# Kernel optimization log

Hardware: AMD Instinct MI355X
Metric: run time of the kernel (lower is better)

The kernel has to match this reference:

```python
import jax, jax.numpy as jnp
import numpy as np

B, N, L = 1, 512, 384
D_IN, D_OUT, HEADS, D_FF = 128, 64, 4, 256
EPS = 1e-5


def layer_norm(x, g, b):
    m = jnp.mean(x, axis=-1, keepdims=True)
    v = jnp.mean((x - m) ** 2, axis=-1, keepdims=True)
    return g * (x - m) / jnp.sqrt(v + EPS) + b


def setup_inputs() -> dict:
    key = jax.random.key(0)
    ks = jax.random.split(key, 10)
    s = 0.05
    return {
        "src": jax.random.normal(ks[0], (B, L, L, D_IN), jnp.float32),
        "tgt": jax.random.normal(ks[1], (B, N, L, D_OUT), jnp.float32),
        "Wp": jax.random.normal(ks[2], (D_IN, HEADS), jnp.float32) * s,
        "bp": jnp.zeros((HEADS,), jnp.float32),
        "Wm": jax.random.normal(ks[3], (D_OUT, D_OUT), jnp.float32) * s,
        "bm": jnp.zeros((D_OUT,), jnp.float32),
        "Wo": jax.random.normal(ks[4], (D_OUT, D_OUT), jnp.float32) * s,
        "bo": jnp.zeros((D_OUT,), jnp.float32),
        "W1": jax.random.normal(ks[5], (D_OUT, D_FF), jnp.float32) * s,
        "b1": jnp.zeros((D_FF,), jnp.float32),
        "W2": jax.random.normal(ks[6], (D_FF, D_OUT), jnp.float32) * s,
        "b2": jnp.zeros((D_OUT,), jnp.float32),
        "g_norm": jnp.ones((D_IN,), jnp.float32),
        "bt_norm": jnp.zeros((D_IN,), jnp.float32),
        "g1": jnp.ones((D_OUT,), jnp.float32),
        "bt1": jnp.zeros((D_OUT,), jnp.float32),
        "g2": jnp.ones((D_OUT,), jnp.float32),
        "bt2": jnp.zeros((D_OUT,), jnp.float32),
    }


def reference(src, tgt, Wp, bp, Wm, bm, Wo, bo, W1, b1, W2, b2,
              g_norm, bt_norm, g1, bt1, g2, bt2):
    H = HEADS
    C = D_OUT // H  # channels per head group
    # symmetrize pair features over the two residue axes
    src = 0.5 * (src + jnp.swapaxes(src, 1, 2))
    src = layer_norm(src, g_norm, bt_norm)
    tgt2 = layer_norm(tgt, g1, bt1)
    # attention map from pair features; softmax over the FIRST residue axis (dim=1)
    attn = jax.nn.softmax(src @ Wp + bp, axis=1)          # [B, L(k), L(l), H]
    # value projection of MSA, split channels into (C, H) matching view(B,-1,H,N,L)
    v = (tgt2 @ Wm + bm).reshape(B, N, L, C, H)           # [B, N, L(k), C, H]
    # out[b,n,l,c,h] = sum_k v[b,n,k,c,h] * attn[b,k,l,h]
    o = jnp.einsum('bnkch,bklh->bnlch', v, attn).reshape(B, N, L, D_OUT)
    tgt2 = o @ Wo + bo
    tgt = tgt + tgt2
    # norm2 (view to (B*N,L,-1) is irrelevant: LN acts on last dim) + FFN
    tgt2 = layer_norm(tgt, g2, bt2)
    tgt2 = jax.nn.relu(tgt2 @ W1 + b1) @ W2 + b2
    return tgt + tgt2
```

## Files before the change

### kernel.cpp

```cpp
#include <hip/hip_runtime.h>
#include <math.h>

#define LL 384
#define NN 512
#define DIN 128
#define DOUT 64
#define HH 4
#define CC 16
#define DFF 256
#define EPS 1e-5f

typedef __attribute__((ext_vector_type(4))) float f32x4;
typedef __attribute__((ext_vector_type(8))) short bf16x8;

__device__ __forceinline__ short f2bf(float f) {
    union { float f; unsigned u; } v; v.f = f;
    unsigned r = v.u + 0x7fff + ((v.u >> 16) & 1);
    return (short)(r >> 16);
}
#define MFMA16(a, b, c) __builtin_amdgcn_mfma_f32_16x16x32_bf16(a, b, c, 0, 0, 0)

__global__ __launch_bounds__(256) void k1_logits(
    const float* __restrict__ src, const float* __restrict__ Wp,
    const float* __restrict__ bp, const float* __restrict__ g_norm,
    const float* __restrict__ bt_norm, float* __restrict__ logits)
{
    int k = blockIdx.x;
    int wave = threadIdx.x >> 6;
    int lane = threadIdx.x & 63;
    int l = blockIdx.y * 4 + wave;
    if (k > l) return;
    const float* r1 = src + ((size_t)k * LL + l) * DIN;
    const float* r2 = src + ((size_t)l * LL + k) * DIN;
    float2 a = *(const float2*)(r1 + lane * 2);
    float2 b = *(const float2*)(r2 + lane * 2);
    float x0 = 0.5f * (a.x + b.x);
    float x1 = 0.5f * (a.y + b.y);
    float s = x0 + x1, ss = x0 * x0 + x1 * x1;
    #pragma unroll
    for (int m = 1; m < 64; m <<= 1) { s += __shfl_xor(s, m); ss += __shfl_xor(ss, m); }
    float mean = s * (1.0f / DIN);
    float var  = ss * (1.0f / DIN) - mean * mean;
    float rstd = rsqrtf(var + EPS);
    int d0 = lane * 2;
    float n0 = g_norm[d0]     * (x0 - mean) * rstd + bt_norm[d0];
    float n1 = g_norm[d0 + 1] * (x1 - mean) * rstd + bt_norm[d0 + 1];
    float4 w0 = *(const float4*)(Wp + d0 * HH);
    float4 w1 = *(const float4*)(Wp + d0 * HH + HH);
    float p0 = n0 * w0.x + n1 * w1.x;
    float p1 = n0 * w0.y + n1 * w1.y;
    float p2 = n0 * w0.z + n1 * w1.z;
    float p3 = n0 * w0.w + n1 * w1.w;
    #pragma unroll
    for (int m = 1; m < 64; m <<= 1) {
        p0 += __shfl_xor(p0, m); p1 += __shfl_xor(p1, m);
        p2 += __shfl_xor(p2, m); p3 += __shfl_xor(p3, m);
    }
    int hh = lane & 3;
    float pv = (hh == 0 ? p0 : hh == 1 ? p1 : hh == 2 ? p2 : p3) + bp[hh];
    if (lane < 4)                 logits[((size_t)l * HH + hh) * LL + k] = pv;
    else if (lane < 8 && k != l)  logits[((size_t)k * HH + hh) * LL + l] = pv;
}

__global__ __launch_bounds__(256) void k2_softmax(
    const float* __restrict__ logits, short* __restrict__ attn_bf)
{
    int l = blockIdx.x;
    int h = threadIdx.x >> 6;
    int lane = threadIdx.x & 63;
    const float* row = logits + ((size_t)l * HH + h) * LL;
    float v[6];
    float mx = -1e30f;
    #pragma unroll
    for (int j = 0; j < 6; j++) { v[j] = row[lane + 64 * j]; mx = fmaxf(mx, v[j]); }
    #pragma unroll
    for (int m = 1; m < 64; m <<= 1) mx = fmaxf(mx, __shfl_xor(mx, m));
    float sum = 0.f;
    #pragma unroll
    for (int j = 0; j < 6; j++) { v[j] = __expf(v[j] - mx); sum += v[j]; }
    #pragma unroll
    for (int m = 1; m < 64; m <<= 1) sum += __shfl_xor(sum, m);
    float inv = 1.0f / sum;
    short* orow = attn_bf + ((size_t)h * LL + l) * LL;
    #pragma unroll
    for (int j = 0; j < 6; j++) orow[lane + 64 * j] = f2bf(v[j] * inv);
}

__global__ __launch_bounds__(256) void k3_v(
    const float* __restrict__ tgt, const float* __restrict__ Wm,
    const float* __restrict__ bm, const float* __restrict__ g1,
    const float* __restrict__ bt1, short* __restrict__ vt_bf)
{
    int tid = threadIdx.x, wave = tid >> 6, lane = tid & 63;
    int c15 = lane & 15, g = lane >> 4;
    bf16x8 wb[2][4];
    #pragma unroll
    for (int kf = 0; kf < 2; kf++)
        #pragma unroll
        for (int nt = 0; nt < 4; nt++) {
            bf16x8 w;
            #pragma unroll
            for (int i = 0; i < 8; i++) {
                int k = kf * 32 + g * 8 + i;
                w[i] = f2bf(Wm[k * DOUT + c15 * HH + nt]);
            }
            wb[kf][nt] = w;
        }
    float bmr[4];
    #pragma unroll
    for (int nt = 0; nt < 4; nt++) bmr[nt] = bm[c15 * HH + nt];
    float g1a[8], g1b[8], bta[8], btb[8];
    #pragma unroll
    for (int i = 0; i < 8; i++) {
        g1a[i] = g1[g * 8 + i];       bta[i] = bt1[g * 8 + i];
        g1b[i] = g1[32 + g * 8 + i];  btb[i] = bt1[32 + g * 8 + i];
    }
    const f32x4 zero = {0.f, 0.f, 0.f, 0.f};
    int gwave = blockIdx.x * 4 + wave;
    int nwaves = gridDim.x * 4;
    const int NT = NN * LL / 16;
    for (int t = gwave; t < NT; t += nwaves) {
        int r0 = t * 16;
        const float* tb = tgt + (size_t)r0 * DOUT + c15 * DOUT + g * 8;
        float4 xa = *(const float4*)(tb);
        float4 xb = *(const float4*)(tb + 4);
        float4 xc = *(const float4*)(tb + 32);
        float4 xd = *(const float4*)(tb + 36);
        float ya[8] = {xa.x, xa.y, xa.z, xa.w, xb.x, xb.y, xb.z, xb.w};
        float yb[8] = {xc.x, xc.y, xc.z, xc.w, xd.x, xd.y, xd.z, xd.w};
        float s = 0.f, ss = 0.f;
        #pragma unroll
        for (int i = 0; i < 8; i++) {
            s += ya[i] + yb[i];
            ss += ya[i] * ya[i] + yb[i] * yb[i];
        }
        s  += __shfl_xor(s, 16);  s  += __shfl_xor(s, 32);
        ss += __shfl_xor(ss, 16); ss += __shfl_xor(ss, 32);
        float mean = s * (1.0f / DOUT);
        float var  = ss * (1.0f / DOUT) - mean * mean;
        float rstd = rsqrtf(var + EPS);
        bf16x8 a0, a1;
        #pragma unroll
        for (int i = 0; i < 8; i++) {
            a0[i] = f2bf(g1a[i] * (ya[i] - mean) * rstd + bta[i]);
            a1[i] = f2bf(g1b[i] * (yb[i] - mean) * rstd + btb[i]);
        }
        f32x4 acc[4];
        #pragma unroll
        for (int nt = 0; nt < 4; nt++) {
            acc[nt] = MFMA16(a0, wb[0][nt], zero);
            acc[nt] = MFMA16(a1, wb[1][nt], acc[nt]);
        }
        int n = r0 / LL, k0 = r0 % LL;
        #pragma unroll
        for (int nt = 0; nt < 4; nt++)
            #pragma unroll
            for (int j = 0; j < 4; j++) {
                int k = k0 + g * 4 + j;
                vt_bf[((size_t)(nt * LL + k)) * (NN * CC) + n * CC + c15] =
                    f2bf(acc[nt][j] + bmr[nt]);
            }
    }
}

#define K4S 56
__global__ __launch_bounds__(256) void k4_mfma(
    const short* __restrict__ attn_bf, const short* __restrict__ vt_bf,
    short* __restrict__ o_bf)
{
    __shared__ short As[LL * K4S];
    __shared__ short Bs[64 * K4S];
    int h = blockIdx.y;
    int m0 = blockIdx.x * 64;
    int tid = threadIdx.x, wave = tid >> 6, lane = tid & 63;
    int c15 = lane & 15, g = lane >> 4;
    f32x4 acc[6][4];
    #pragma unroll
    for (int i = 0; i < 6; i++)
        #pragma unroll
        for (int nt = 0; nt < 4; nt++) acc[i][nt] = (f32x4){0.f, 0.f, 0.f, 0.f};

    for (int k0 = 0; k0 < LL; k0 += 32) {
        __syncthreads();
        #pragma unroll
        for (int it = 0; it < 6; it++) {
            int e = tid + 256 * it;
            int l = e >> 2, k8 = (e & 3) * 8;
            bf16x8 v = *(const bf16x8*)(attn_bf + ((size_t)(h * LL + l)) * LL + k0 + k8);
            *(bf16x8*)(As + l * K4S + k8) = v;
        }
        {
            int m = tid & 63, kg = tid >> 6;
            const short* vb = vt_bf + ((size_t)(h * LL + k0 + kg * 8)) * (NN * CC) + m0 + m;
            short tmp[8];
            #pragma unroll
            for (int j = 0; j < 8; j++) tmp[j] = vb[(size_t)j * (NN * CC)];
            #pragma unroll
            for (int j = 0; j < 4; j++) {
                int v2 = (int)(unsigned short)tmp[2 * j] | ((int)(unsigned short)tmp[2 * j + 1] << 16);
                *(int*)(Bs + m * K4S + kg * 8 + 2 * j) = v2;
            }
        }
        __syncthreads();
        bf16x8 bfr[4];
        #pragma unroll
        for (int nt = 0; nt < 4; nt++)
            bfr[nt] = *(const bf16x8*)(Bs + (nt * 16 + c15) * K4S + g * 8);
        #pragma unroll
        for (int i = 0; i < 6; i++) {
            int l = (wave + 4 * i) * 16 + c15;
            bf16x8 afr = *(const bf16x8*)(As + l * K4S + g * 8);
            #pragma unroll
            for (int nt = 0; nt < 4; nt++)
                acc[i][nt] = MFMA16(afr, bfr[nt], acc[i][nt]);
        }
    }
    #pragma unroll
    for (int i = 0; i < 6; i++) {
        int l = (wave + 4 * i) * 16 + g * 4;
        #pragma unroll
        for (int nt = 0; nt < 4; nt++) {
            int n = (m0 >> 4) + nt;
            #pragma unroll
            for (int r = 0; r < 4; r++)
                o_bf[((size_t)n * LL + l + r) * DOUT + h * 16 + c15] = f2bf(acc[i][nt][r]);
        }
    }
}

#define W1TS 72
#define W2TS 264
#define K5_LDS ((DFF * W1TS + DOUT * W2TS + 8 * 16 * W2TS) * 2)
__global__ __launch_bounds__(512) void k5_tail(
    const short* __restrict__ o_bf, const float* __restrict__ tgt,
    const float* __restrict__ Wo, const float* __restrict__ bo,
    const float* __restrict__ W1, const float* __restrict__ b1,
    const float* __restrict__ W2, const float* __restrict__ b2,
    const float* __restrict__ g2, const float* __restrict__ bt2,
    float* __restrict__ out)
{
    extern __shared__ short smem[];
    short* W1T = smem;
    short* W2T = W1T + DFF * W1TS;
    short* Fl  = W2T + DOUT * W2TS;
    int tid = threadIdx.x, wave = tid >> 6, lane = tid & 63;
    int c15 = lane & 15, g = lane >> 4;

    for (int e = tid; e < DOUT * DFF; e += 512) {
        int k = e >> 8, p = e & 255;
        W1T[p * W1TS + k] = f2bf(W1[e]);
        int k2 = e >> 6, n = e & 63;
        W2T[n * W2TS + k2] = f2bf(W2[e]);
    }
    bf16x8 woB[2][4];
    #pragma unroll
    for (int kf = 0; kf < 2; kf++)
        #pragma unroll
        for (int nt = 0; nt < 4; nt++) {
            bf16x8 w;
            #pragma unroll
            for (int i2 = 0; i2 < 8; i2++) {
                int k = kf * 32 + g * 8 + i2;
                int rj = (k & 15) * 4 + (k >> 4);
                w[i2] = f2bf(Wo[rj * DOUT + nt * 16 + c15]);
            }
            woB[kf][nt] = w;
        }
    float bor[4], b2r[4], g2r[4], bt2r[4], b1r[16];
    #pragma unroll
    for (int nt = 0; nt < 4; nt++) {
        bor[nt]  = bo[nt * 16 + c15];  b2r[nt]  = b2[nt * 16 + c15];
        g2r[nt]  = g2[nt * 16 + c15];  bt2r[nt] = bt2[nt * 16 + c15];
    }
    #pragma unroll
    for (int nt = 0; nt < 16; nt++) b1r[nt] = b1[nt * 16 + c15];
    __syncthreads();

    short* Fw = Fl + wave * 16 * W2TS;
    int gwave = blockIdx.x * 8 + wave;
    const f32x4 zero = {0.f, 0.f, 0.f, 0.f};

    for (int it = 0; it < 6; it++) {
        int r0 = (gwave * 6 + it) * 16;
        const short* ob = o_bf + (size_t)r0 * DOUT;
        bf16x8 oa0 = *(const bf16x8*)(ob + c15 * DOUT + g * 8);
        bf16x8 oa1 = *(const bf16x8*)(ob + c15 * DOUT + 32 + g * 8);
        f32x4 X[4];
        #pragma unroll
        for (int nt = 0; nt < 4; nt++) {
            X[nt] = MFMA16(oa0, woB[0][nt], zero);
            X[nt] = MFMA16(oa1, woB[1][nt], X[nt]);
        }
        const float* tb = tgt + (size_t)r0 * DOUT;
        #pragma unroll
        for (int nt = 0; nt < 4; nt++)
            #pragma unroll
            for (int j = 0; j < 4; j++)
                X[nt][j] += tb[(g * 4 + j) * DOUT + nt * 16 + c15] + bor[nt];
        #pragma unroll
        for (int j = 0; j < 4; j++) {
            float s  = X[0][j] + X[1][j] + X[2][j] + X[3][j];
            float ss = X[0][j]*X[0][j] + X[1][j]*X[1][j] + X[2][j]*X[2][j] + X[3][j]*X[3][j];
            #pragma unroll
            for (int m = 1; m < 16; m <<= 1) { s += __shfl_xor(s, m); ss += __shfl_xor(ss, m); }
            float mean = s * (1.0f / DOUT);
            float var  = ss * (1.0f / DOUT) - mean * mean;
            float rstd = rsqrtf(var + EPS);
            #pragma unroll
            for (int nt = 0; nt < 4; nt++) {
                float y = g2r[nt] * (X[nt][j] - mean) * rstd + bt2r[nt];
                Fw[(g * 4 + j) * W2TS + nt * 16 + c15] = f2bf(y);
            }
        }
        bf16x8 ya0 = *(const bf16x8*)(Fw + c15 * W2TS + g * 8);
        bf16x8 ya1 = *(const bf16x8*)(Fw + c15 * W2TS + 32 + g * 8);
        f32x4 Fa[16];
        #pragma unroll
        for (int nt = 0; nt < 16; nt++) {
            bf16x8 wb0 = *(const bf16x8*)(W1T + (nt * 16 + c15) * W1TS + g * 8);
            bf16x8 wb1 = *(const bf16x8*)(W1T + (nt * 16 + c15) * W1TS + 32 + g * 8);
            Fa[nt] = MFMA16(ya0, wb0, zero);
            Fa[nt] = MFMA16(ya1, wb1, Fa[nt]);
        }
        #pragma unroll
        for (int nt = 0; nt < 16; nt++)
            #pragma unroll
            for (int j = 0; j < 4; j++)
                Fw[(g * 4 + j) * W2TS + nt * 16 + c15] = f2bf(fmaxf(Fa[nt][j] + b1r[nt], 0.f));
        bf16x8 fa[8];
        #pragma unroll
        for (int kf = 0; kf < 8; kf++)
            fa[kf] = *(const bf16x8*)(Fw + c15 * W2TS + kf * 32 + g * 8);
        #pragma unroll
        for (int nt = 0; nt < 4; nt++)
            #pragma unroll
            for (int kf = 0; kf < 8; kf++) {
                bf16x8 wb = *(const bf16x8*)(W2T + (nt * 16 + c15) * W2TS + kf * 32 + g * 8);
                X[nt] = MFMA16(fa[kf], wb, X[nt]);
            }
        float* outb = out + (size_t)r0 * DOUT;
        #pragma unroll
        for (int nt = 0; nt < 4; nt++)
            #pragma unroll
            for (int j = 0; j < 4; j++)
                outb[(g * 4 + j) * DOUT + nt * 16 + c15] = X[nt][j] + b2r[nt];
    }
}

extern "C" void kernel_launch(void* const* d_in, const int* in_sizes, int n_in,
                              void* d_out, int out_size, void* d_ws, size_t ws_size,
                              hipStream_t stream)
{
    (void)in_sizes; (void)n_in; (void)out_size; (void)ws_size;
    const float* src     = (const float*)d_in[0];
    const float* tgt     = (const float*)d_in[1];
    const float* Wp      = (const float*)d_in[2];
    const float* bp      = (const float*)d_in[3];
    const float* Wm      = (const float*)d_in[4];
    const float* bm      = (const float*)d_in[5];
    const float* Wo      = (const float*)d_in[6];
    const float* bo      = (const float*)d_in[7];
    const float* W1      = (const float*)d_in[8];
    const float* b1      = (const float*)d_in[9];
    const float* W2      = (const float*)d_in[10];
    const float* b2      = (const float*)d_in[11];
    const float* g_norm  = (const float*)d_in[12];
    const float* bt_norm = (const float*)d_in[13];
    const float* g1      = (const float*)d_in[14];
    const float* bt1     = (const float*)d_in[15];
    const float* g2      = (const float*)d_in[16];
    const float* bt2     = (const float*)d_in[17];
    float* out = (float*)d_out;
    float* ws  = (float*)d_ws;

    float* logits  = ws;
    short* attn_bf = (short*)(ws + 589824);
    short* vt_bf   = attn_bf + 589824;
    short* o_bf    = vt_bf + 12582912;

    hipFuncSetAttribute((const void*)k5_tail,
                        hipFuncAttributeMaxDynamicSharedMemorySize, K5_LDS);

    k1_logits <<<dim3(LL, LL / 4), 256, 0, stream>>>(src, Wp, bp, g_norm, bt_norm, logits);
    k2_softmax<<<LL, 256, 0, stream>>>(logits, attn_bf);
    k3_v      <<<1024, 256, 0, stream>>>(tgt, Wm, bm, g1, bt1, vt_bf);
    k4_mfma   <<<dim3((NN * CC) / 64, HH), 256, 0, stream>>>(attn_bf, vt_bf, o_bf);
    k5_tail   <<<256, 512, K5_LDS, stream>>>(o_bf, tgt, Wo, bo, W1, b1, W2, b2, g2, bt2, out);
}
```

Before: 284.4 us.

## Halve k4 N-tile, swizzle k5 LDS layout, prefetch next tile inputs in k5

The attention-value GEMM kernel now uses 32-column tiles instead of 64. That doubles its grid size and cuts LDS padding and accumulator registers, at the cost of reloading the attention tile twice as often. The tail kernel drops padded LDS strides in favour of an XOR swizzle to avoid bank conflicts. It also software-prefetches the next row-block's o and tgt values into registers to hide global load latency. These changes raise register pressure in k5 and add redundant attention-tile traffic in k4.

```diff
diff --git a/kernel.cpp b/kernel.cpp
--- a/kernel.cpp
+++ b/kernel.cpp
@@ -163,22 +163,22 @@
     }
 }
 
-#define K4S 56
+#define K4S 40
 __global__ __launch_bounds__(256) void k4_mfma(
     const short* __restrict__ attn_bf, const short* __restrict__ vt_bf,
     short* __restrict__ o_bf)
 {
     __shared__ short As[LL * K4S];
-    __shared__ short Bs[64 * K4S];
+    __shared__ short Bs[32 * K4S];
     int h = blockIdx.y;
-    int m0 = blockIdx.x * 64;
+    int m0 = blockIdx.x * 32;
     int tid = threadIdx.x, wave = tid >> 6, lane = tid & 63;
     int c15 = lane & 15, g = lane >> 4;
-    f32x4 acc[6][4];
+    f32x4 acc[6][2];
     #pragma unroll
     for (int i = 0; i < 6; i++)
         #pragma unroll
-        for (int nt = 0; nt < 4; nt++) acc[i][nt] = (f32x4){0.f, 0.f, 0.f, 0.f};
+        for (int nt = 0; nt < 2; nt++) acc[i][nt] = (f32x4){0.f, 0.f, 0.f, 0.f};
 
     for (int k0 = 0; k0 < LL; k0 += 32) {
         __syncthreads();
@@ -190,28 +190,28 @@
             *(bf16x8*)(As + l * K4S + k8) = v;
         }
         {
-            int m = tid & 63, kg = tid >> 6;
-            const short* vb = vt_bf + ((size_t)(h * LL + k0 + kg * 8)) * (NN * CC) + m0 + m;
-            short tmp[8];
-            #pragma unroll
-            for (int j = 0; j < 8; j++) tmp[j] = vb[(size_t)j * (NN * CC)];
-            #pragma unroll
-            for (int j = 0; j < 4; j++) {
+            int m = tid & 31, kg = tid >> 5;
+            const short* vb = vt_bf + ((size_t)(h * LL + k0 + kg * 4)) * (NN * CC) + m0 + m;
+            short tmp[4];
+            #pragma unroll
+            for (int j = 0; j < 4; j++) tmp[j] = vb[(size_t)j * (NN * CC)];
+            #pragma unroll
+            for (int j = 0; j < 2; j++) {
                 int v2 = (int)(unsigned short)tmp[2 * j] | ((int)(unsigned short)tmp[2 * j + 1] << 16);
-                *(int*)(Bs + m * K4S + kg * 8 + 2 * j) = v2;
+                *(int*)(Bs + m * K4S + kg * 4 + 2 * j) = v2;
             }
         }
         __syncthreads();
-        bf16x8 bfr[4];
-        #pragma unroll
-        for (int nt = 0; nt < 4; nt++)
+        bf16x8 bfr[2];
+        #pragma unroll
+        for (int nt = 0; nt < 2; nt++)
             bfr[nt] = *(const bf16x8*)(Bs + (nt * 16 + c15) * K4S + g * 8);
         #pragma unroll
         for (int i = 0; i < 6; i++) {
             int l = (wave + 4 * i) * 16 + c15;
             bf16x8 afr = *(const bf16x8*)(As + l * K4S + g * 8);
             #pragma unroll
-            for (int nt = 0; nt < 4; nt++)
+            for (int nt = 0; nt < 2; nt++)
                 acc[i][nt] = MFMA16(afr, bfr[nt], acc[i][nt]);
         }
     }
@@ -219,7 +219,7 @@
     for (int i = 0; i < 6; i++) {
         int l = (wave + 4 * i) * 16 + g * 4;
         #pragma unroll
-        for (int nt = 0; nt < 4; nt++) {
+        for (int nt = 0; nt < 2; nt++) {
             int n = (m0 >> 4) + nt;
             #pragma unroll
             for (int r = 0; r < 4; r++)
@@ -228,9 +228,8 @@
     }
 }
 
-#define W1TS 72
-#define W2TS 264
-#define K5_LDS ((DFF * W1TS + DOUT * W2TS + 8 * 16 * W2TS) * 2)
+#define SWZ(col, row) ((col) ^ (((row) & 7) << 3))
+#define K5_LDS ((DFF * 64 + DOUT * 256 + 8 * 16 * 256) * 2)
 __global__ __launch_bounds__(512) void k5_tail(
     const short* __restrict__ o_bf, const float* __restrict__ tgt,
     const float* __restrict__ Wo, const float* __restrict__ bo,
@@ -241,16 +240,16 @@
 {
     extern __shared__ short smem[];
     short* W1T = smem;
-    short* W2T = W1T + DFF * W1TS;
-    short* Fl  = W2T + DOUT * W2TS;
+    short* W2T = W1T + DFF * 64;
+    short* Fl  = W2T + DOUT * 256;
     int tid = threadIdx.x, wave = tid >> 6, lane = tid & 63;
     int c15 = lane & 15, g = lane >> 4;
 
     for (int e = tid; e < DOUT * DFF; e += 512) {
         int k = e >> 8, p = e & 255;
-        W1T[p * W1TS + k] = f2bf(W1[e]);
+        W1T[p * 64 + SWZ(k, p)] = f2bf(W1[e]);
         int k2 = e >> 6, n = e & 63;
-        W2T[n * W2TS + k2] = f2bf(W2[e]);
+        W2T[n * 256 + SWZ(k2, n)] = f2bf(W2[e]);
     }
     bf16x8 woB[2][4];
     #pragma unroll
@@ -276,27 +275,43 @@
     for (int nt = 0; nt < 16; nt++) b1r[nt] = b1[nt * 16 + c15];
     __syncthreads();
 
-    short* Fw = Fl + wave * 16 * W2TS;
+    short* Fw = Fl + wave * 16 * 256;
     int gwave = blockIdx.x * 8 + wave;
     const f32x4 zero = {0.f, 0.f, 0.f, 0.f};
 
+    int r0c = (gwave * 6) * 16;
+    bf16x8 oa0 = *(const bf16x8*)(o_bf + (size_t)r0c * DOUT + c15 * DOUT + g * 8);
+    bf16x8 oa1 = *(const bf16x8*)(o_bf + (size_t)r0c * DOUT + c15 * DOUT + 32 + g * 8);
+    float tg[16];
+    #pragma unroll
+    for (int nt = 0; nt < 4; nt++)
+        #pragma unroll
+        for (int j = 0; j < 4; j++)
+            tg[nt * 4 + j] = tgt[(size_t)r0c * DOUT + (g * 4 + j) * DOUT + nt * 16 + c15];
+
     for (int it = 0; it < 6; it++) {
-        int r0 = (gwave * 6 + it) * 16;
-        const short* ob = o_bf + (size_t)r0 * DOUT;
-        bf16x8 oa0 = *(const bf16x8*)(ob + c15 * DOUT + g * 8);
-        bf16x8 oa1 = *(const bf16x8*)(ob + c15 * DOUT + 32 + g * 8);
+        int r0 = r0c;
+        int r0n = (it < 5) ? (gwave * 6 + it + 1) * 16 : r0c;
+        bf16x8 noa0 = *(const bf16x8*)(o_bf + (size_t)r0n * DOUT + c15 * DOUT + g * 8);
+        bf16x8 noa1 = *(const bf16x8*)(o_bf + (size_t)r0n * DOUT + c15 * DOUT + 32 + g * 8);
+        float ntg[16];
+        #pragma unroll
+        for (int nt = 0; nt < 4; nt++)
+            #pragma unroll
+            for (int j = 0; j < 4; j++)
+                ntg[nt * 4 + j] = tgt[(size_t)r0n * DOUT + (g * 4 + j) * DOUT + nt * 16 + c15];
+
         f32x4 X[4];
         #pragma unroll
         for (int nt = 0; nt < 4; nt++) {
             X[nt] = MFMA16(oa0, woB[0][nt], zero);
             X[nt] = MFMA16(oa1, woB[1][nt], X[nt]);
         }
-        const float* tb = tgt + (size_t)r0 * DOUT;
         #pragma unroll
         for (int nt = 0; nt < 4; nt++)
             #pragma unroll
             for (int j = 0; j < 4; j++)
-                X[nt][j] += tb[(g * 4 + j) * DOUT + nt * 16 + c15] + bor[nt];
+                X[nt][j] += tg[nt * 4 + j] + bor[nt];
         #pragma unroll
         for (int j = 0; j < 4; j++) {
             float s  = X[0][j] + X[1][j] + X[2][j] + X[3][j];
@@ -306,36 +321,41 @@
             float mean = s * (1.0f / DOUT);
             float var  = ss * (1.0f / DOUT) - mean * mean;
             float rstd = rsqrtf(var + EPS);
+            int row = g * 4 + j;
             #pragma unroll
             for (int nt = 0; nt < 4; nt++) {
                 float y = g2r[nt] * (X[nt][j] - mean) * rstd + bt2r[nt];
-                Fw[(g * 4 + j) * W2TS + nt * 16 + c15] = f2bf(y);
-            }
-        }
-        bf16x8 ya0 = *(const bf16x8*)(Fw + c15 * W2TS + g * 8);
-        bf16x8 ya1 = *(const bf16x8*)(Fw + c15 * W2TS + 32 + g * 8);
+                Fw[row * 256 + SWZ(nt * 16 + c15, row)] = f2bf(y);
+            }
+        }
+        bf16x8 ya0 = *(const bf16x8*)(Fw + c15 * 256 + SWZ(g * 8, c15));
+        bf16x8 ya1 = *(const bf16x8*)(Fw + c15 * 256 + SWZ(32 + g * 8, c15));
         f32x4 Fa[16];
         #pragma unroll
         for (int nt = 0; nt < 16; nt++) {
-            bf16x8 wb0 = *(const bf16x8*)(W1T + (nt * 16 + c15) * W1TS + g * 8);
-            bf16x8 wb1 = *(const bf16x8*)(W1T + (nt * 16 + c15) * W1TS + 32 + g * 8);
+            int row = nt * 16 + c15;
+            bf16x8 wb0 = *(const bf16x8*)(W1T + row * 64 + SWZ(g * 8, row));
+            bf16x8 wb1 = *(const bf16x8*)(W1T + row * 64 + SWZ(32 + g * 8, row));
             Fa[nt] = MFMA16(ya0, wb0, zero);
             Fa[nt] = MFMA16(ya1, wb1, Fa[nt]);
         }
         #pragma unroll
         for (int nt = 0; nt < 16; nt++)
             #pragma unroll
-            for (int j = 0; j < 4; j++)
-                Fw[(g * 4 + j) * W2TS + nt * 16 + c15] = f2bf(fmaxf(Fa[nt][j] + b1r[nt], 0.f));
+            for (int j = 0; j < 4; j++) {
+                int row = g * 4 + j;
+                Fw[row * 256 + SWZ(nt * 16 + c15, row)] = f2bf(fmaxf(Fa[nt][j] + b1r[nt], 0.f));
+            }
         bf16x8 fa[8];
         #pragma unroll
         for (int kf = 0; kf < 8; kf++)
-            fa[kf] = *(const bf16x8*)(Fw + c15 * W2TS + kf * 32 + g * 8);
+            fa[kf] = *(const bf16x8*)(Fw + c15 * 256 + SWZ(kf * 32 + g * 8, c15));
         #pragma unroll
         for (int nt = 0; nt < 4; nt++)
             #pragma unroll
             for (int kf = 0; kf < 8; kf++) {
-                bf16x8 wb = *(const bf16x8*)(W2T + (nt * 16 + c15) * W2TS + kf * 32 + g * 8);
+                int row = nt * 16 + c15;
+                bf16x8 wb = *(const bf16x8*)(W2T + row * 256 + SWZ(kf * 32 + g * 8, row));
                 X[nt] = MFMA16(fa[kf], wb, X[nt]);
             }
         float* outb = out + (size_t)r0 * DOUT;
@@ -344,6 +364,11 @@
             #pragma unroll
             for (int j = 0; j < 4; j++)
                 outb[(g * 4 + j) * DOUT + nt * 16 + c15] = X[nt][j] + b2r[nt];
+
+        oa0 = noa0; oa1 = noa1;
+        #pragma unroll
+        for (int q = 0; q < 16; q++) tg[q] = ntg[q];
+        r0c = r0n;
     }
 }
 
@@ -384,6 +409,6 @@
     k1_logits <<<dim3(LL, LL / 4), 256, 0, stream>>>(src, Wp, bp, g_norm, bt_norm, logits);
     k2_softmax<<<LL, 256, 0, stream>>>(logits, attn_bf);
     k3_v      <<<1024, 256, 0, stream>>>(tgt, Wm, bm, g1, bt1, vt_bf);
-    k4_mfma   <<<dim3((NN * CC) / 64, HH), 256, 0, stream>>>(attn_bf, vt_bf, o_bf);
+    k4_mfma   <<<dim3((NN * CC) / 32, HH), 256, 0, stream>>>(attn_bf, vt_bf, o_bf);
     k5_tail   <<<256, 512, K5_LDS, stream>>>(o_bf, tgt, Wo, bo, W1, b1, W2, b2, g2, bt2, out);
 }
```

Measured after the change: 315.7 us. +11.0%, slower.
